# Kernel tuning notes

Hardware: AMD Instinct MI355X
Metric: run time of the kernel (lower is better)

The kernel has to match this reference:

```python
import jax, jax.numpy as jnp
import numpy as np

B, S, D, H = 2, 2048, 2048, 16
HD = D // H


def setup_inputs() -> dict:
    key = jax.random.key(0)
    kx, = jax.random.split(key, 1)
    return {
        "x": jax.random.normal(kx, (B, S, D), dtype=jnp.float32),
        "q_mask": jnp.ones((D, D), dtype=jnp.float32),
        "k_mask": jnp.ones((D, D), dtype=jnp.float32),
        "v_mask": jnp.ones((D, D), dtype=jnp.float32),
        "out_mask": jnp.ones((D, D), dtype=jnp.float32),
        "head_mask": jnp.ones((H,), dtype=jnp.float32),
        "attention_mask": jnp.ones((B, S), dtype=jnp.float32),
        "shared_weight": jnp.float32(1.0),
    }


def reference(x, q_mask, k_mask, v_mask, out_mask, head_mask, attention_mask, shared_weight):
    b, s, d = x.shape
    scale = jnp.float32(HD) ** -0.5

    def shared_linear(inp, mask):
        # F.linear(x, mask * shared_weight): out = inp @ (mask*sw).T
        return jnp.einsum("bsd,ed->bse", inp, mask * shared_weight)

    q = shared_linear(x, q_mask).reshape(b, s, H, HD).transpose(0, 2, 1, 3)  # [B,H,S,HD]
    k = shared_linear(x, k_mask).reshape(b, s, H, HD).transpose(0, 2, 1, 3)
    v = shared_linear(x, v_mask).reshape(b, s, H, HD).transpose(0, 2, 1, 3)

    hm = head_mask.reshape(1, H, 1, 1)
    q, k, v = q * hm, k * hm, v * hm

    scores = jnp.einsum("bhqd,bhkd->bhqk", q, k) * scale  # [B,H,S,S]

    # causal mask: upper triangle (j > i) -> -inf
    causal = jnp.triu(jnp.ones((s, s), dtype=bool), k=1)
    scores = jnp.where(causal, -jnp.inf, scores)

    # additive attention mask: (1 - m) * -10000, broadcast [B,1,1,S]
    scores = scores + (1.0 - attention_mask)[:, None, None, :] * -10000.0

    attn = jax.nn.softmax(scores, axis=-1)  # dropout is identity in eval / p=0

    out = jnp.einsum("bhqk,bhkd->bhqd", attn, v)          # [B,H,S,HD]
    out = out.transpose(0, 2, 1, 3).reshape(b, s, d)       # [B,S,D]
    return shared_linear(out, out_mask)
```

## Files before the change

### kernel.cpp

```cpp
#include <hip/hip_runtime.h>

#define B_  2
#define S_  2048
#define D_  2048
#define H_  16
#define HD_ 128

typedef __bf16 bf16;
typedef __bf16 bf16x4 __attribute__((ext_vector_type(4)));
typedef __bf16 bf16x8 __attribute__((ext_vector_type(8)));
typedef float  f32x4  __attribute__((ext_vector_type(4)));

__device__ __forceinline__ void gld_lds16(const void* g, void* l) {
    __builtin_amdgcn_global_load_lds(
        (const __attribute__((address_space(1))) unsigned int*)g,
        (__attribute__((address_space(3))) unsigned int*)l, 16, 0, 0);
}

__device__ __forceinline__ f32x4 mfma16(bf16x8 a, bf16x8 b, f32x4 c) {
    return __builtin_amdgcn_mfma_f32_16x16x32_bf16(a, b, c, 0, 0, 0);
}

#define BAR()        do { __builtin_amdgcn_s_barrier(); asm volatile("" ::: "memory"); } while (0)
#define WAIT_LGKM0() do { asm volatile("s_waitcnt lgkmcnt(0)" ::: "memory"); \
                          __builtin_amdgcn_sched_barrier(0); } while (0)

__global__ __launch_bounds__(256)
void precast_kernel(const float* __restrict__ x, bf16* __restrict__ xh,
                    bf16* __restrict__ xl) {
    int i = (blockIdx.x * 256 + threadIdx.x) * 8;
    float4 a = *(const float4*)(x + i);
    float4 b = *(const float4*)(x + i + 4);
    float av[8] = {a.x, a.y, a.z, a.w, b.x, b.y, b.z, b.w};
    bf16x8 h8, l8;
#pragma unroll
    for (int e = 0; e < 8; e++) {
        bf16 hv = (bf16)av[e];
        h8[e] = hv;
        l8[e] = (bf16)(av[e] - (float)hv);
    }
    *(bf16x8*)(xh + i) = h8;
    *(bf16x8*)(xl + i) = l8;
}

__global__ __launch_bounds__(256)
void precast_mask(const float* __restrict__ s0, bf16* __restrict__ d0,
                  const float* __restrict__ s1, bf16* __restrict__ d1,
                  const float* __restrict__ swp) {
    const float sw = swp[0];
    int bid = blockIdx.x;
    const float* src = s0; bf16* dst = d0;
    if (bid >= 2048) { src = s1; dst = d1; bid -= 2048; }
    int i = (bid * 256 + threadIdx.x) * 8;
    float4 a = *(const float4*)(src + i);
    float4 b = *(const float4*)(src + i + 4);
    bf16x8 o;
    o[0] = (bf16)(a.x * sw); o[1] = (bf16)(a.y * sw);
    o[2] = (bf16)(a.z * sw); o[3] = (bf16)(a.w * sw);
    o[4] = (bf16)(b.x * sw); o[5] = (bf16)(b.y * sw);
    o[6] = (bf16)(b.z * sw); o[7] = (bf16)(b.w * sw);
    *(bf16x8*)(dst + i) = o;
}

template<int BM, int BN, int WM, int WN, int MODE>
__global__ __launch_bounds__(512)
void gemm8p(const bf16* __restrict__ Ah_g, const bf16* __restrict__ Al_g,
            const bf16* __restrict__ Bq, const bf16* __restrict__ Bk,
            const float* __restrict__ hm,
            bf16* __restrict__ o_qh, bf16* __restrict__ o_ql,
            bf16* __restrict__ o_kh, bf16* __restrict__ o_kl,
            bf16* __restrict__ o_vt, float* __restrict__ o_f32,
            int nt) {
    constexpr int IM = BM / WM / 16;
    constexpr int JN = BN / WN / 16;
    constexpr int IH = IM / 2, JH = JN / 2;
    constexpr int ISSA = BM / 64;
    constexpr int ISSB = BN / 64;
    constexpr int VMW = ISSA + ISSB;
    constexpr int BUFE = (BM + BN) * 64;

    __shared__ bf16 sm[2 * BUFE];

    const int t = threadIdx.x;
    const int wave = t >> 6, lane = t & 63;
    const int lrow = lane & 15, quad = lane >> 4;
    const int wr = wave / WN, wc = wave % WN;
    const int m0 = blockIdx.y * BM, n0 = blockIdx.x * BN;

    const int nsec = (MODE == 0) ? (n0 & (D_ - 1)) : n0;
    const bf16* Bg = (MODE == 0 && n0 >= D_) ? Bk : Bq;

    const int arow = wr * (BM / WM) + lrow;
    const int brow = wc * (BN / WN) + lrow;
    const int g0e = (quad ^ (lrow & 7)) * 8;
    const int g1e = g0e ^ 32;

    auto stage_A = [&](int kt, int p) {
        const bf16* As = (MODE == 0 && kt >= 32) ? Al_g : Ah_g;
        const int kc = ((MODE == 0) ? (kt & 31) : kt) * 64;
        bf16* buf = sm + p * BUFE;
        const int r0 = wave * (BM / 8);
#pragma unroll
        for (int pp = 0; pp < ISSA; pp++) {
            int r = r0 + pp * 8 + (lane >> 3);
            int gc = ((lane & 7) ^ (r & 7)) * 8;
            gld_lds16(As + (size_t)(m0 + r) * D_ + kc + gc,
                      buf + (r0 + pp * 8) * 64);
        }
    };
    auto stage_B = [&](int kt, int p) {
        const int kc = ((MODE == 0) ? (kt & 31) : kt) * 64;
        bf16* buf = sm + p * BUFE + BM * 64;
        const int r0 = wave * (BN / 8);
#pragma unroll
        for (int pp = 0; pp < ISSB; pp++) {
            int r = r0 + pp * 8 + (lane >> 3);
            int gc = ((lane & 7) ^ (r & 7)) * 8;
            gld_lds16(Bg + (size_t)(nsec + r) * D_ + kc + gc,
                      buf + (r0 + pp * 8) * 64);
        }
    };

    f32x4 acc[IM][JN];
#pragma unroll
    for (int i = 0; i < IM; i++)
#pragma unroll
        for (int j = 0; j < JN; j++) acc[i][j] = (f32x4){0.f, 0.f, 0.f, 0.f};

    stage_A(0, 0); stage_B(0, 0);
    stage_A(1, 1); stage_B(1, 1);

    const bf16 *Ab, *Bb;
    auto rdA = [&](int ii, int ge) -> bf16x8 {
        return *(const bf16x8*)&Ab[(arow + ii * 16) * 64 + ge];
    };
    auto rdB = [&](int jj, int ge) -> bf16x8 {
        return *(const bf16x8*)&Bb[(brow + jj * 16) * 64 + ge];
    };

    int p = 0;
    for (int kt = 0; kt < nt; ++kt) {
        if (kt < nt - 1) {
            if constexpr (VMW == 8) asm volatile("s_waitcnt vmcnt(8)" ::: "memory");
            else                    asm volatile("s_waitcnt vmcnt(6)" ::: "memory");
        } else {
            asm volatile("s_waitcnt vmcnt(0)" ::: "memory");
        }
        BAR();
        Ab = sm + p * BUFE;
        Bb = Ab + BM * 64;

        bf16x8 a[IH][2], b[JH][2], b2[JH][2];

#pragma unroll
        for (int i = 0; i < IH; i++) { a[i][0] = rdA(i, g0e); a[i][1] = rdA(i, g1e); }
#pragma unroll
        for (int j = 0; j < JH; j++) { b[j][0] = rdB(j, g0e); b[j][1] = rdB(j, g1e); }
        BAR();
        WAIT_LGKM0();
        __builtin_amdgcn_s_setprio(1);
#pragma unroll
        for (int i = 0; i < IH; i++)
#pragma unroll
            for (int j = 0; j < JH; j++) {
                acc[i][j] = mfma16(a[i][0], b[j][0], acc[i][j]);
                acc[i][j] = mfma16(a[i][1], b[j][1], acc[i][j]);
            }
        __builtin_amdgcn_s_setprio(0);
        BAR();

#pragma unroll
        for (int j = 0; j < JH; j++) { b2[j][0] = rdB(JH + j, g0e); b2[j][1] = rdB(JH + j, g1e); }
        BAR();
        WAIT_LGKM0();
        __builtin_amdgcn_s_setprio(1);
#pragma unroll
        for (int i = 0; i < IH; i++)
#pragma unroll
            for (int j = 0; j < JH; j++) {
                acc[i][JH + j] = mfma16(a[i][0], b2[j][0], acc[i][JH + j]);
                acc[i][JH + j] = mfma16(a[i][1], b2[j][1], acc[i][JH + j]);
            }
        __builtin_amdgcn_s_setprio(0);
        BAR();

        if (kt + 2 < nt) stage_B(kt + 2, p);

#pragma unroll
        for (int i = 0; i < IH; i++) { a[i][0] = rdA(IH + i, g0e); a[i][1] = rdA(IH + i, g1e); }
        BAR();
        WAIT_LGKM0();
        __builtin_amdgcn_s_setprio(1);
#pragma unroll
        for (int i = 0; i < IH; i++)
#pragma unroll
            for (int j = 0; j < JH; j++) {
                acc[IH + i][j] = mfma16(a[i][0], b[j][0], acc[IH + i][j]);
                acc[IH + i][j] = mfma16(a[i][1], b[j][1], acc[IH + i][j]);
            }
        __builtin_amdgcn_s_setprio(0);
        BAR();

        if (kt + 2 < nt) stage_A(kt + 2, p);

        __builtin_amdgcn_s_setprio(1);
#pragma unroll
        for (int i = 0; i < IH; i++)
#pragma unroll
            for (int j = 0; j < JH; j++) {
                acc[IH + i][JH + j] = mfma16(a[i][0], b2[j][0], acc[IH + i][JH + j]);
                acc[IH + i][JH + j] = mfma16(a[i][1], b2[j][1], acc[IH + i][JH + j]);
            }
        __builtin_amdgcn_s_setprio(0);
        p ^= 1;
    }

    if constexpr (MODE == 0) {
        const bool isq = (n0 < D_);
        bf16* oh = isq ? o_qh : o_kh;
        bf16* ol = isq ? o_ql : o_kl;
#pragma unroll
        for (int j = 0; j < JN; j++) {
            int nb = nsec + wc * (BN / WN) + j * 16;
            int h = nb >> 7;
            float hv = hm[h];
#pragma unroll
            for (int i = 0; i < IM; i++) {
                int mB = m0 + wr * (BM / WM) + i * 16 + quad * 4;
                int bb = mB >> 11, s = mB & (S_ - 1);
                size_t idx0 = (((size_t)bb * H_ + h) * S_ + s) * HD_ + (nb & 127) + lrow;
#pragma unroll
                for (int r = 0; r < 4; r++) {
                    float v = acc[i][j][r] * hv;
                    bf16 hvv = (bf16)v;
                    bf16 lvv = (bf16)(v - (float)hvv);
                    oh[idx0 + (size_t)r * HD_] = hvv;
                    ol[idx0 + (size_t)r * HD_] = lvv;
                }
            }
        }
    }
    if constexpr (MODE == 1) {
        __syncthreads();
        bf16* tr = sm;
#pragma unroll
        for (int j = 0; j < JN; j++) {
            int nl = wc * (BN / WN) + j * 16 + lrow;
            float hv = hm[(n0 + nl) >> 7];
#pragma unroll
            for (int i = 0; i < IM; i++) {
                int ml = wr * (BM / WM) + i * 16 + quad * 4;
                bf16x4 pk;
#pragma unroll
                for (int r = 0; r < 4; r++) pk[r] = (bf16)(acc[i][j][r] * hv);
                *(bf16x4*)&tr[nl * 136 + ml] = pk;
            }
        }
        __syncthreads();
        const int bI = m0 >> 11;
        const int s0 = m0 & (S_ - 1);
#pragma unroll
        for (int w = 0; w < 8; w++) {
            int nrow = w * 32 + (t >> 4);
            int c = t & 15;
            bf16x8 vv = *(const bf16x8*)&tr[nrow * 136 + c * 8];
            int ng = n0 + nrow;
            int h = ng >> 7, hd = ng & 127;
            *(bf16x8*)&o_vt[((size_t)(bI * H_ + h) * HD_ + hd) * S_ + s0 + c * 8] = vv;
        }
    }
    if constexpr (MODE == 2) {
#pragma unroll
        for (int j = 0; j < JN; j++) {
            int n = n0 + wc * (BN / WN) + j * 16 + lrow;
#pragma unroll
            for (int i = 0; i < IM; i++) {
                int mB = m0 + wr * (BM / WM) + i * 16 + quad * 4;
#pragma unroll
                for (int r = 0; r < 4; r++)
                    o_f32[(size_t)(mB + r) * D_ + n] = acc[i][j][r];
            }
        }
    }
}

#define SPLD 72

__global__ __launch_bounds__(256, 2)
void attn_kernel(const bf16* __restrict__ qh_, const bf16* __restrict__ ql_,
                 const bf16* __restrict__ kh_, const bf16* __restrict__ kl_,
                 const bf16* __restrict__ vt_, const float* __restrict__ am,
                 bf16* __restrict__ outp) {
    const int bh = blockIdx.x & 31;
    const int qblk = 31 - (blockIdx.x >> 5);
    const int b = bh >> 4, h = bh & 15;
    const int i0 = qblk * 64;
    const int t = threadIdx.x, wave = t >> 6, lane = t & 63;
    const int lrow = lane & 15, quad = lane >> 4;

    __shared__ bf16 skh[64 * 128];
    __shared__ bf16 skl[64 * 128];
    __shared__ bf16 svt[128 * 64];
    __shared__ bf16 sp[4][16 * SPLD];

    const size_t kbase = (size_t)bh * S_ * HD_;
    const size_t vbase = (size_t)bh * HD_ * S_;

    const int qrow = i0 + wave * 16 + lrow;
    bf16x8 qhf[4], qlf[4];
#pragma unroll
    for (int c = 0; c < 4; c++) {
        qhf[c] = *(const bf16x8*)&qh_[kbase + (size_t)qrow * HD_ + c * 32 + quad * 8];
        qlf[c] = *(const bf16x8*)&ql_[kbase + (size_t)qrow * HD_ + c * 32 + quad * 8];
    }

    float m_i[4], l_i[4];
    f32x4 O[8];
#pragma unroll
    for (int r = 0; r < 4; r++) { m_i[r] = -INFINITY; l_i[r] = 0.f; }
#pragma unroll
    for (int n2 = 0; n2 < 8; n2++) O[n2] = (f32x4){0.f, 0.f, 0.f, 0.f};

    const float scale = 0.08838834764831845f;

    for (int j0 = 0; j0 <= i0; j0 += 64) {
        __syncthreads();
#pragma unroll
        for (int p = 0; p < 4; p++) {
            int rb = wave * 16 + p * 4;
            int r = rb + (lane >> 4);
            int gl = ((lane & 15) ^ (r & 7)) * 8;
            gld_lds16(kh_ + kbase + (size_t)(j0 + r) * HD_ + gl, &skh[rb * 128]);
            gld_lds16(kl_ + kbase + (size_t)(j0 + r) * HD_ + gl, &skl[rb * 128]);
        }
#pragma unroll
        for (int p = 0; p < 4; p++) {
            int db = wave * 32 + p * 8;
            int d = db + (lane >> 3);
            int gl = ((lane & 7) ^ (d & 7)) * 8;
            gld_lds16(vt_ + vbase + (size_t)d * S_ + j0 + gl, &svt[db * 64]);
        }
        __syncthreads();

        float amadd[4];
#pragma unroll
        for (int nt = 0; nt < 4; nt++)
            amadd[nt] = (1.0f - am[b * S_ + j0 + nt * 16 + lrow]) * -10000.0f;

        f32x4 s4[4];
#pragma unroll
        for (int nt = 0; nt < 4; nt++) s4[nt] = (f32x4){0.f, 0.f, 0.f, 0.f};
#pragma unroll
        for (int c = 0; c < 4; c++) {
#pragma unroll
            for (int nt = 0; nt < 4; nt++) {
                int ka = (nt * 16 + lrow) * 128 + (((c * 4 + quad) ^ (lrow & 7)) * 8);
                bf16x8 kb8 = *(const bf16x8*)&skh[ka];
                bf16x8 lb8 = *(const bf16x8*)&skl[ka];
                s4[nt] = __builtin_amdgcn_mfma_f32_16x16x32_bf16(qhf[c], kb8, s4[nt], 0, 0, 0);
                s4[nt] = __builtin_amdgcn_mfma_f32_16x16x32_bf16(qhf[c], lb8, s4[nt], 0, 0, 0);
                s4[nt] = __builtin_amdgcn_mfma_f32_16x16x32_bf16(qlf[c], kb8, s4[nt], 0, 0, 0);
            }
        }

        const bool diag = (j0 == i0);
#pragma unroll
        for (int r = 0; r < 4; r++) {
            const int rrow = wave * 16 + quad * 4 + r;
            float sv[4], pw[4];
            float mx = -INFINITY;
#pragma unroll
            for (int nt = 0; nt < 4; nt++) {
                float xv = s4[nt][r] * scale + amadd[nt];
                if (diag && (nt * 16 + lrow) > rrow) xv = -INFINITY;
                sv[nt] = xv;
                mx = fmaxf(mx, xv);
            }
#pragma unroll
            for (int off = 1; off < 16; off <<= 1) mx = fmaxf(mx, __shfl_xor(mx, off));
            float mnew = fmaxf(m_i[r], mx);
            float alpha = __expf(m_i[r] - mnew);
            float ps = 0.f;
#pragma unroll
            for (int nt = 0; nt < 4; nt++) { pw[nt] = __expf(sv[nt] - mnew); ps += pw[nt]; }
#pragma unroll
            for (int off = 1; off < 16; off <<= 1) ps += __shfl_xor(ps, off);
            l_i[r] = l_i[r] * alpha + ps;
            m_i[r] = mnew;
#pragma unroll
            for (int n2 = 0; n2 < 8; n2++) O[n2][r] *= alpha;
#pragma unroll
            for (int nt = 0; nt < 4; nt++)
                sp[wave][(quad * 4 + r) * SPLD + nt * 16 + lrow] = (bf16)pw[nt];
        }
        __asm__ volatile("s_waitcnt lgkmcnt(0)" ::: "memory");

#pragma unroll
        for (int k2 = 0; k2 < 2; k2++) {
            bf16x8 pf = *(const bf16x8*)&sp[wave][lrow * SPLD + k2 * 32 + quad * 8];
            const int gp = ((quad + k2 * 4) ^ (lrow & 7)) * 8;
#pragma unroll
            for (int n2 = 0; n2 < 8; n2++) {
                bf16x8 vf8 = *(const bf16x8*)&svt[(n2 * 16 + lrow) * 64 + gp];
                O[n2] = __builtin_amdgcn_mfma_f32_16x16x32_bf16(pf, vf8, O[n2], 0, 0, 0);
            }
        }
    }

    float inv[4];
#pragma unroll
    for (int r = 0; r < 4; r++) inv[r] = 1.0f / l_i[r];
#pragma unroll
    for (int n2 = 0; n2 < 8; n2++)
#pragma unroll
        for (int r = 0; r < 4; r++) {
            int srow = i0 + wave * 16 + quad * 4 + r;
            outp[((size_t)(b * S_ + srow)) * D_ + h * HD_ + n2 * 16 + lrow] =
                (bf16)(O[n2][r] * inv[r]);
        }
}

extern "C" void kernel_launch(void* const* d_in, const int* in_sizes, int n_in,
                              void* d_out, int out_size, void* d_ws, size_t ws_size,
                              hipStream_t stream) {
    const float* x  = (const float*)d_in[0];
    const float* qm = (const float*)d_in[1];
    const float* km = (const float*)d_in[2];
    const float* vm = (const float*)d_in[3];
    const float* om = (const float*)d_in[4];
    const float* hm = (const float*)d_in[5];
    const float* am = (const float*)d_in[6];
    const float* sw = (const float*)d_in[7];
    float* out = (float*)d_out;

    const size_t P = (size_t)B_ * H_ * S_ * HD_ * sizeof(bf16);
    char* ws = (char*)d_ws;
    bf16* xh = (bf16*)(ws + 0 * P);
    bf16* xl = (bf16*)(ws + 1 * P);
    bf16* qh = (bf16*)(ws + 2 * P);
    bf16* ql = (bf16*)(ws + 3 * P);
    bf16* kh = (bf16*)(ws + 4 * P);
    bf16* kl = (bf16*)(ws + 5 * P);
    bf16* attn_out = xh;
    bf16* vmb = xl;
    bf16* omb = qh;
    bf16* vt  = (bf16*)d_out;
    bf16* qmb = (bf16*)((char*)d_out + 16u * 1024 * 1024);
    bf16* kmb = (bf16*)((char*)d_out + 24u * 1024 * 1024);

    precast_kernel<<<(B_ * S_ * D_) / (256 * 8), 256, 0, stream>>>(x, xh, xl);
    precast_mask<<<4096, 256, 0, stream>>>(qm, qmb, km, kmb, sw);

    gemm8p<256, 256, 2, 4, 0><<<dim3(16, 16), 512, 0, stream>>>(
        xh, xl, qmb, kmb, hm, qh, ql, kh, kl, nullptr, nullptr, 64);

    precast_mask<<<2048, 256, 0, stream>>>(vm, vmb, nullptr, nullptr, sw);
    gemm8p<128, 256, 2, 4, 1><<<dim3(8, 32), 512, 0, stream>>>(
        xh, nullptr, vmb, nullptr, hm,
        nullptr, nullptr, nullptr, nullptr, vt, nullptr, 32);

    attn_kernel<<<1024, 256, 0, stream>>>(qh, ql, kh, kl, vt, am, attn_out);

    precast_mask<<<2048, 256, 0, stream>>>(om, omb, nullptr, nullptr, sw);
    gemm8p<256, 128, 4, 2, 2><<<dim3(16, 16), 512, 0, stream>>>(
        attn_out, nullptr, omb, nullptr, hm,
        nullptr, nullptr, nullptr, nullptr, nullptr, out, 32);
}
```

Before: 491.5 us.

## Rewrite GEMMs as 256-thread two-occupancy kernels and register-prefetch attention K/V

Replaces the 512-thread 8-wave GEMM with a 256-thread 4-wave kernel that uses K-step 32, smaller tiles, a new LDS swizzle, two workgroups per CU and an XCD-aware block remap. The attention kernel now prefetches the next K/V tile into registers while computing the current one, instead of doing synchronous global-to-LDS loads. The aim is better occupancy, L2 locality and load/compute overlap. The cost is more loop iterations, more barriers per FLOP and higher register pressure in the attention kernel.

```diff
diff --git a/kernel.cpp b/kernel.cpp
--- a/kernel.cpp
+++ b/kernel.cpp
@@ -10,6 +10,7 @@
 typedef __bf16 bf16x4 __attribute__((ext_vector_type(4)));
 typedef __bf16 bf16x8 __attribute__((ext_vector_type(8)));
 typedef float  f32x4  __attribute__((ext_vector_type(4)));
+typedef unsigned int u32x4 __attribute__((ext_vector_type(4)));
 
 __device__ __forceinline__ void gld_lds16(const void* g, void* l) {
     __builtin_amdgcn_global_load_lds(
@@ -21,7 +22,7 @@
     return __builtin_amdgcn_mfma_f32_16x16x32_bf16(a, b, c, 0, 0, 0);
 }
 
-#define BAR()        do { __builtin_amdgcn_s_barrier(); asm volatile("" ::: "memory"); } while (0)
+#define BAR()        asm volatile("s_barrier" ::: "memory")
 #define WAIT_LGKM0() do { asm volatile("s_waitcnt lgkmcnt(0)" ::: "memory"); \
                           __builtin_amdgcn_sched_barrier(0); } while (0)
 
@@ -62,62 +63,65 @@
     *(bf16x8*)(dst + i) = o;
 }
 
-template<int BM, int BN, int WM, int WN, int MODE>
-__global__ __launch_bounds__(512)
-void gemm8p(const bf16* __restrict__ Ah_g, const bf16* __restrict__ Al_g,
+template<int BM, int BN, int MODE>
+__global__ __launch_bounds__(256, 2)
+void gemm2p(const bf16* __restrict__ Ah_g, const bf16* __restrict__ Al_g,
             const bf16* __restrict__ Bq, const bf16* __restrict__ Bk,
             const float* __restrict__ hm,
             bf16* __restrict__ o_qh, bf16* __restrict__ o_ql,
             bf16* __restrict__ o_kh, bf16* __restrict__ o_kl,
             bf16* __restrict__ o_vt, float* __restrict__ o_f32,
             int nt) {
-    constexpr int IM = BM / WM / 16;
-    constexpr int JN = BN / WN / 16;
-    constexpr int IH = IM / 2, JH = JN / 2;
+    constexpr int IM = BM / 2 / 16;
+    constexpr int JN = BN / 2 / 16;
+    constexpr int IH = IM / 2;
     constexpr int ISSA = BM / 64;
     constexpr int ISSB = BN / 64;
-    constexpr int VMW = ISSA + ISSB;
-    constexpr int BUFE = (BM + BN) * 64;
-
-    __shared__ bf16 sm[2 * BUFE];
+    constexpr int BUFE = (BM + BN) * 32;
+    constexpr int SMELEMS = (MODE == 1 && BN * (BM + 8) > 2 * BUFE)
+                                ? BN * (BM + 8) : 2 * BUFE;
+    __shared__ bf16 sm[SMELEMS];
 
     const int t = threadIdx.x;
     const int wave = t >> 6, lane = t & 63;
     const int lrow = lane & 15, quad = lane >> 4;
-    const int wr = wave / WN, wc = wave % WN;
-    const int m0 = blockIdx.y * BM, n0 = blockIdx.x * BN;
+    const int wr = wave >> 1, wc = wave & 1;
+
+    const int gx = gridDim.x;
+    const int id0 = blockIdx.y * gx + blockIdx.x;
+    const int nwg = gx * gridDim.y;
+    const int id = (id0 & 7) * (nwg >> 3) + (id0 >> 3);
+    const int m0 = (id / gx) * BM, n0 = (id % gx) * BN;
 
     const int nsec = (MODE == 0) ? (n0 & (D_ - 1)) : n0;
     const bf16* Bg = (MODE == 0 && n0 >= D_) ? Bk : Bq;
 
-    const int arow = wr * (BM / WM) + lrow;
-    const int brow = wc * (BN / WN) + lrow;
-    const int g0e = (quad ^ (lrow & 7)) * 8;
-    const int g1e = g0e ^ 32;
-
-    auto stage_A = [&](int kt, int p) {
-        const bf16* As = (MODE == 0 && kt >= 32) ? Al_g : Ah_g;
-        const int kc = ((MODE == 0) ? (kt & 31) : kt) * 64;
-        bf16* buf = sm + p * BUFE;
-        const int r0 = wave * (BM / 8);
+    const int arow = wr * (BM / 2) + lrow;
+    const int brow = wc * (BN / 2) + lrow;
+    const int gsw = (quad ^ ((lrow >> 1) & 3)) * 8;
+
+    const int srr = lane >> 2, spg = lane & 3;
+    const int ssw = (spg ^ ((srr >> 1) & 3)) * 8;
+
+    auto stage_A = [&](int kt, int pbuf) {
+        const bf16* As = (MODE == 0 && kt >= 64) ? Al_g : Ah_g;
+        const int kc = ((MODE == 0) ? (kt & 63) : kt) * 32;
+        bf16* buf = sm + pbuf * BUFE;
 #pragma unroll
         for (int pp = 0; pp < ISSA; pp++) {
-            int r = r0 + pp * 8 + (lane >> 3);
-            int gc = ((lane & 7) ^ (r & 7)) * 8;
-            gld_lds16(As + (size_t)(m0 + r) * D_ + kc + gc,
-                      buf + (r0 + pp * 8) * 64);
+            int r0 = wave * (BM / 4) + pp * 16;
+            gld_lds16(As + (size_t)(m0 + r0 + srr) * D_ + kc + ssw,
+                      buf + r0 * 32);
         }
     };
-    auto stage_B = [&](int kt, int p) {
-        const int kc = ((MODE == 0) ? (kt & 31) : kt) * 64;
-        bf16* buf = sm + p * BUFE + BM * 64;
-        const int r0 = wave * (BN / 8);
+    auto stage_B = [&](int kt, int pbuf) {
+        const int kc = ((MODE == 0) ? (kt & 63) : kt) * 32;
+        bf16* buf = sm + pbuf * BUFE + BM * 32;
 #pragma unroll
         for (int pp = 0; pp < ISSB; pp++) {
-            int r = r0 + pp * 8 + (lane >> 3);
-            int gc = ((lane & 7) ^ (r & 7)) * 8;
-            gld_lds16(Bg + (size_t)(nsec + r) * D_ + kc + gc,
-                      buf + (r0 + pp * 8) * 64);
+            int r0 = wave * (BN / 4) + pp * 16;
+            gld_lds16(Bg + (size_t)(nsec + r0 + srr) * D_ + kc + ssw,
+                      buf + r0 * 32);
         }
     };
 
@@ -127,90 +131,48 @@
 #pragma unroll
         for (int j = 0; j < JN; j++) acc[i][j] = (f32x4){0.f, 0.f, 0.f, 0.f};
 
-    stage_A(0, 0); stage_B(0, 0);
-    stage_A(1, 1); stage_B(1, 1);
-
-    const bf16 *Ab, *Bb;
-    auto rdA = [&](int ii, int ge) -> bf16x8 {
-        return *(const bf16x8*)&Ab[(arow + ii * 16) * 64 + ge];
-    };
-    auto rdB = [&](int jj, int ge) -> bf16x8 {
-        return *(const bf16x8*)&Bb[(brow + jj * 16) * 64 + ge];
-    };
+    stage_A(0, 0); stage_B(0, 0); stage_B(1, 1);
 
     int p = 0;
     for (int kt = 0; kt < nt; ++kt) {
-        if (kt < nt - 1) {
-            if constexpr (VMW == 8) asm volatile("s_waitcnt vmcnt(8)" ::: "memory");
-            else                    asm volatile("s_waitcnt vmcnt(6)" ::: "memory");
-        } else {
-            asm volatile("s_waitcnt vmcnt(0)" ::: "memory");
-        }
+        if (kt < nt - 1) asm volatile("s_waitcnt vmcnt(2)" ::: "memory");
+        else             asm volatile("s_waitcnt vmcnt(0)" ::: "memory");
         BAR();
-        Ab = sm + p * BUFE;
-        Bb = Ab + BM * 64;
-
-        bf16x8 a[IH][2], b[JH][2], b2[JH][2];
-
-#pragma unroll
-        for (int i = 0; i < IH; i++) { a[i][0] = rdA(i, g0e); a[i][1] = rdA(i, g1e); }
-#pragma unroll
-        for (int j = 0; j < JH; j++) { b[j][0] = rdB(j, g0e); b[j][1] = rdB(j, g1e); }
+        if (kt + 1 < nt) stage_A(kt + 1, p ^ 1);
+
+        const bf16* Ab = sm + p * BUFE;
+        const bf16* Bb = Ab + BM * 32;
+        bf16x8 a[IH], b[JN];
+
+#pragma unroll
+        for (int j = 0; j < JN; j++)
+            b[j] = *(const bf16x8*)&Bb[(brow + j * 16) * 32 + gsw];
+#pragma unroll
+        for (int i = 0; i < IH; i++)
+            a[i] = *(const bf16x8*)&Ab[(arow + i * 16) * 32 + gsw];
         BAR();
         WAIT_LGKM0();
         __builtin_amdgcn_s_setprio(1);
 #pragma unroll
         for (int i = 0; i < IH; i++)
 #pragma unroll
-            for (int j = 0; j < JH; j++) {
-                acc[i][j] = mfma16(a[i][0], b[j][0], acc[i][j]);
-                acc[i][j] = mfma16(a[i][1], b[j][1], acc[i][j]);
-            }
+            for (int j = 0; j < JN; j++)
+                acc[i][j] = mfma16(a[i], b[j], acc[i][j]);
         __builtin_amdgcn_s_setprio(0);
         BAR();
 
-#pragma unroll
-        for (int j = 0; j < JH; j++) { b2[j][0] = rdB(JH + j, g0e); b2[j][1] = rdB(JH + j, g1e); }
-        BAR();
+        if (kt + 2 < nt) stage_B(kt + 2, p);
+
+#pragma unroll
+        for (int i = 0; i < IH; i++)
+            a[i] = *(const bf16x8*)&Ab[(arow + (IH + i) * 16) * 32 + gsw];
         WAIT_LGKM0();
         __builtin_amdgcn_s_setprio(1);
 #pragma unroll
         for (int i = 0; i < IH; i++)
 #pragma unroll
-            for (int j = 0; j < JH; j++) {
-                acc[i][JH + j] = mfma16(a[i][0], b2[j][0], acc[i][JH + j]);
-                acc[i][JH + j] = mfma16(a[i][1], b2[j][1], acc[i][JH + j]);
-            }
-        __builtin_amdgcn_s_setprio(0);
-        BAR();
-
-        if (kt + 2 < nt) stage_B(kt + 2, p);
-
-#pragma unroll
-        for (int i = 0; i < IH; i++) { a[i][0] = rdA(IH + i, g0e); a[i][1] = rdA(IH + i, g1e); }
-        BAR();
-        WAIT_LGKM0();
-        __builtin_amdgcn_s_setprio(1);
-#pragma unroll
-        for (int i = 0; i < IH; i++)
-#pragma unroll
-            for (int j = 0; j < JH; j++) {
-                acc[IH + i][j] = mfma16(a[i][0], b[j][0], acc[IH + i][j]);
-                acc[IH + i][j] = mfma16(a[i][1], b[j][1], acc[IH + i][j]);
-            }
-        __builtin_amdgcn_s_setprio(0);
-        BAR();
-
-        if (kt + 2 < nt) stage_A(kt + 2, p);
-
-        __builtin_amdgcn_s_setprio(1);
-#pragma unroll
-        for (int i = 0; i < IH; i++)
-#pragma unroll
-            for (int j = 0; j < JH; j++) {
-                acc[IH + i][JH + j] = mfma16(a[i][0], b2[j][0], acc[IH + i][JH + j]);
-                acc[IH + i][JH + j] = mfma16(a[i][1], b2[j][1], acc[IH + i][JH + j]);
-            }
+            for (int j = 0; j < JN; j++)
+                acc[IH + i][j] = mfma16(a[i], b[j], acc[IH + i][j]);
         __builtin_amdgcn_s_setprio(0);
         p ^= 1;
     }
@@ -221,12 +183,12 @@
         bf16* ol = isq ? o_ql : o_kl;
 #pragma unroll
         for (int j = 0; j < JN; j++) {
-            int nb = nsec + wc * (BN / WN) + j * 16;
+            int nb = nsec + wc * (BN / 2) + j * 16;
             int h = nb >> 7;
             float hv = hm[h];
 #pragma unroll
             for (int i = 0; i < IM; i++) {
-                int mB = m0 + wr * (BM / WM) + i * 16 + quad * 4;
+                int mB = m0 + wr * (BM / 2) + i * 16 + quad * 4;
                 int bb = mB >> 11, s = mB & (S_ - 1);
                 size_t idx0 = (((size_t)bb * H_ + h) * S_ + s) * HD_ + (nb & 127) + lrow;
 #pragma unroll
@@ -245,11 +207,11 @@
         bf16* tr = sm;
 #pragma unroll
         for (int j = 0; j < JN; j++) {
-            int nl = wc * (BN / WN) + j * 16 + lrow;
+            int nl = wc * (BN / 2) + j * 16 + lrow;
             float hv = hm[(n0 + nl) >> 7];
 #pragma unroll
             for (int i = 0; i < IM; i++) {
-                int ml = wr * (BM / WM) + i * 16 + quad * 4;
+                int ml = wr * (BM / 2) + i * 16 + quad * 4;
                 bf16x4 pk;
 #pragma unroll
                 for (int r = 0; r < 4; r++) pk[r] = (bf16)(acc[i][j][r] * hv);
@@ -261,7 +223,7 @@
         const int s0 = m0 & (S_ - 1);
 #pragma unroll
         for (int w = 0; w < 8; w++) {
-            int nrow = w * 32 + (t >> 4);
+            int nrow = w * 16 + (t >> 4);
             int c = t & 15;
             bf16x8 vv = *(const bf16x8*)&tr[nrow * 136 + c * 8];
             int ng = n0 + nrow;
@@ -272,10 +234,10 @@
     if constexpr (MODE == 2) {
 #pragma unroll
         for (int j = 0; j < JN; j++) {
-            int n = n0 + wc * (BN / WN) + j * 16 + lrow;
+            int n = n0 + wc * (BN / 2) + j * 16 + lrow;
 #pragma unroll
             for (int i = 0; i < IM; i++) {
-                int mB = m0 + wr * (BM / WM) + i * 16 + quad * 4;
+                int mB = m0 + wr * (BM / 2) + i * 16 + quad * 4;
 #pragma unroll
                 for (int r = 0; r < 4; r++)
                     o_f32[(size_t)(mB + r) * D_ + n] = acc[i][j][r];
@@ -314,33 +276,56 @@
         qlf[c] = *(const bf16x8*)&ql_[kbase + (size_t)qrow * HD_ + c * 32 + quad * 8];
     }
 
-    float m_i[4], l_i[4];
-    f32x4 O[8];
-#pragma unroll
-    for (int r = 0; r < 4; r++) { m_i[r] = -INFINITY; l_i[r] = 0.f; }
-#pragma unroll
-    for (int n2 = 0; n2 < 8; n2++) O[n2] = (f32x4){0.f, 0.f, 0.f, 0.f};
-
-    const float scale = 0.08838834764831845f;
-
-    for (int j0 = 0; j0 <= i0; j0 += 64) {
-        __syncthreads();
+    u32x4 kpre[8], vpre[4];
+    auto issueKV = [&](int j0) {
 #pragma unroll
         for (int p = 0; p < 4; p++) {
             int rb = wave * 16 + p * 4;
             int r = rb + (lane >> 4);
             int gl = ((lane & 15) ^ (r & 7)) * 8;
-            gld_lds16(kh_ + kbase + (size_t)(j0 + r) * HD_ + gl, &skh[rb * 128]);
-            gld_lds16(kl_ + kbase + (size_t)(j0 + r) * HD_ + gl, &skl[rb * 128]);
+            kpre[p]     = *(const u32x4*)(kh_ + kbase + (size_t)(j0 + r) * HD_ + gl);
+            kpre[4 + p] = *(const u32x4*)(kl_ + kbase + (size_t)(j0 + r) * HD_ + gl);
         }
 #pragma unroll
         for (int p = 0; p < 4; p++) {
             int db = wave * 32 + p * 8;
             int d = db + (lane >> 3);
             int gl = ((lane & 7) ^ (d & 7)) * 8;
-            gld_lds16(vt_ + vbase + (size_t)d * S_ + j0 + gl, &svt[db * 64]);
-        }
-        __syncthreads();
+            vpre[p] = *(const u32x4*)(vt_ + vbase + (size_t)d * S_ + j0 + gl);
+        }
+    };
+    auto writeKV = [&]() {
+#pragma unroll
+        for (int p = 0; p < 4; p++) {
+            int rb = wave * 16 + p * 4;
+            *(u32x4*)&skh[rb * 128 + lane * 8] = kpre[p];
+            *(u32x4*)&skl[rb * 128 + lane * 8] = kpre[4 + p];
+        }
+#pragma unroll
+        for (int p = 0; p < 4; p++) {
+            int db = wave * 32 + p * 8;
+            *(u32x4*)&svt[db * 64 + lane * 8] = vpre[p];
+        }
+    };
+
+    float m_i[4], l_i[4];
+    f32x4 O[8];
+#pragma unroll
+    for (int r = 0; r < 4; r++) { m_i[r] = -INFINITY; l_i[r] = 0.f; }
+#pragma unroll
+    for (int n2 = 0; n2 < 8; n2++) O[n2] = (f32x4){0.f, 0.f, 0.f, 0.f};
+
+    const float scale = 0.08838834764831845f;
+
+    issueKV(0);
+
+    for (int j0 = 0; j0 <= i0; j0 += 64) {
+        asm volatile("s_waitcnt vmcnt(0)" ::: "memory");
+        BAR();
+        writeKV();
+        if (j0 + 64 <= i0) issueKV(j0 + 64);
+        asm volatile("s_waitcnt lgkmcnt(0)" ::: "memory");
+        BAR();
 
         float amadd[4];
 #pragma unroll
@@ -357,9 +342,9 @@
                 int ka = (nt * 16 + lrow) * 128 + (((c * 4 + quad) ^ (lrow & 7)) * 8);
                 bf16x8 kb8 = *(const bf16x8*)&skh[ka];
                 bf16x8 lb8 = *(const bf16x8*)&skl[ka];
-                s4[nt] = __builtin_amdgcn_mfma_f32_16x16x32_bf16(qhf[c], kb8, s4[nt], 0, 0, 0);
-                s4[nt] = __builtin_amdgcn_mfma_f32_16x16x32_bf16(qhf[c], lb8, s4[nt], 0, 0, 0);
-                s4[nt] = __builtin_amdgcn_mfma_f32_16x16x32_bf16(qlf[c], kb8, s4[nt], 0, 0, 0);
+                s4[nt] = mfma16(qhf[c], kb8, s4[nt]);
+                s4[nt] = mfma16(qhf[c], lb8, s4[nt]);
+                s4[nt] = mfma16(qlf[c], kb8, s4[nt]);
             }
         }
 
@@ -393,7 +378,7 @@
             for (int nt = 0; nt < 4; nt++)
                 sp[wave][(quad * 4 + r) * SPLD + nt * 16 + lrow] = (bf16)pw[nt];
         }
-        __asm__ volatile("s_waitcnt lgkmcnt(0)" ::: "memory");
+        asm volatile("s_waitcnt lgkmcnt(0)" ::: "memory");
 
 #pragma unroll
         for (int k2 = 0; k2 < 2; k2++) {
@@ -402,7 +387,7 @@
 #pragma unroll
             for (int n2 = 0; n2 < 8; n2++) {
                 bf16x8 vf8 = *(const bf16x8*)&svt[(n2 * 16 + lrow) * 64 + gp];
-                O[n2] = __builtin_amdgcn_mfma_f32_16x16x32_bf16(pf, vf8, O[n2], 0, 0, 0);
+                O[n2] = mfma16(pf, vf8, O[n2]);
             }
         }
     }
@@ -448,21 +433,21 @@
     bf16* qmb = (bf16*)((char*)d_out + 16u * 1024 * 1024);
     bf16* kmb = (bf16*)((char*)d_out + 24u * 1024 * 1024);
 
-    precast_kernel<<<(B_ * S_ * D_) / (256 * 8), 256, 0, stream>>>(x, xh, xl);
+    precast_kernel<<<4096, 256, 0, stream>>>(x, xh, xl);
     precast_mask<<<4096, 256, 0, stream>>>(qm, qmb, km, kmb, sw);
 
-    gemm8p<256, 256, 2, 4, 0><<<dim3(16, 16), 512, 0, stream>>>(
-        xh, xl, qmb, kmb, hm, qh, ql, kh, kl, nullptr, nullptr, 64);
+    gemm2p<256, 128, 0><<<dim3(32, 16), 256, 0, stream>>>(
+        xh, xl, qmb, kmb, hm, qh, ql, kh, kl, nullptr, nullptr, 128);
 
     precast_mask<<<2048, 256, 0, stream>>>(vm, vmb, nullptr, nullptr, sw);
-    gemm8p<128, 256, 2, 4, 1><<<dim3(8, 32), 512, 0, stream>>>(
+    gemm2p<128, 128, 1><<<dim3(16, 32), 256, 0, stream>>>(
         xh, nullptr, vmb, nullptr, hm,
-        nullptr, nullptr, nullptr, nullptr, vt, nullptr, 32);
+        nullptr, nullptr, nullptr, nullptr, vt, nullptr, 64);
 
     attn_kernel<<<1024, 256, 0, stream>>>(qh, ql, kh, kl, vt, am, attn_out);
 
     precast_mask<<<2048, 256, 0, stream>>>(om, omb, nullptr, nullptr, sw);
-    gemm8p<256, 128, 4, 2, 2><<<dim3(16, 16), 512, 0, stream>>>(
+    gemm2p<128, 128, 2><<<dim3(16, 32), 256, 0, stream>>>(
         attn_out, nullptr, omb, nullptr, hm,
-        nullptr, nullptr, nullptr, nullptr, nullptr, out, 32);
-}
+        nullptr, nullptr, nullptr, nullptr, nullptr, out, 64);
+}
```

New measurement: 491.5 us. No clear change (+0.0%).
